# Kernel optimization log

Hardware: AMD Instinct MI355X
Metric: run time of the kernel (lower is better)

The kernel has to match this reference:

```python
import jax, jax.numpy as jnp
import numpy as np
import math

B, D, DCONV = 8192, 1024, 4
MIN_TS, MAX_TS = 10.0, 2000.0


def setup_inputs() -> dict:
    key = jax.random.key(0)
    ks = jax.random.split(key, 9)
    s_in = 1.0 / math.sqrt(D)
    return {
        "x": jax.random.normal(ks[0], (B, D), jnp.float32),
        "h": jax.random.normal(ks[1], (B, D), jnp.float32),
        "conv_buf": jax.random.normal(ks[2], (B, D, DCONV), jnp.float32),
        "W_in": jax.random.uniform(ks[3], (2 * D, D), jnp.float32, -s_in, s_in),
        "b_in": jax.random.uniform(ks[4], (2 * D,), jnp.float32, -s_in, s_in),
        "conv_w": jax.random.uniform(ks[5], (D, DCONV), jnp.float32, -0.5, 0.5),
        "conv_b": jax.random.uniform(ks[6], (D,), jnp.float32, -0.5, 0.5),
        "W_out": jax.random.uniform(ks[7], (D, D), jnp.float32, -s_in, s_in),
        "b_out": jax.random.uniform(ks[8], (D,), jnp.float32, -s_in, s_in),
    }


def _decay(d_model):
    # tau = exp(linspace(log(min_ts), log(max_ts), D)); decay = exp(-1/tau)
    tau = jnp.exp(jnp.linspace(math.log(MIN_TS), math.log(MAX_TS), d_model))
    return jnp.exp(-1.0 / tau)


def reference(x, h, conv_buf, W_in, b_in, conv_w, conv_b, W_out, b_out):
    # in_proj: [B,D] -> [B,2D], split into inner stream and gate
    xz = x @ W_in.T + b_in
    x_inner, z = jnp.split(xz, 2, axis=-1)  # [B,D], [B,D]
    # ring-buffer roll + write newest sample at last slot
    new_buf = jnp.concatenate([conv_buf[:, :, 1:], x_inner[:, :, None]], axis=-1)  # [B,D,K]
    # depthwise conv over the K-window, output length 1
    conv_out = jnp.einsum("bdk,dk->bd", new_buf, conv_w) + conv_b
    conv_out = jax.nn.silu(conv_out)
    # decay-gated recurrence
    decay = _decay(x.shape[-1])
    h_new = decay * h + (1.0 - decay) * conv_out
    # SiLU gate + output projection (dropout is identity in eval)
    out = (h_new * jax.nn.silu(z)) @ W_out.T + b_out
    return out, h_new, new_buf
```

## Files before the change

### kernel.cpp

```cpp
#include <hip/hip_runtime.h>
#include <hip/hip_bf16.h>


typedef float  floatx4 __attribute__((ext_vector_type(4)));
typedef __bf16 bf16x8  __attribute__((ext_vector_type(8)));
typedef unsigned short u16;
typedef unsigned short u16x8 __attribute__((ext_vector_type(8)));

__device__ __forceinline__ float bf2f(u16 u) {
    union { unsigned int i; float f; } v; v.i = ((unsigned int)u) << 16; return v.f;
}
__device__ __forceinline__ u16 f2bf(float f) {
    union { float ff; unsigned int i; } v; v.ff = f;
    return (u16)((v.i + 0x7fffu + ((v.i >> 16) & 1u)) >> 16);
}
__device__ __forceinline__ float silu_f(float x) { return x / (1.f + __expf(-x)); }

#define D_SZ 1024
#define B_SZ 8192
#define ELEMS 8388608
#define WI_ELEMS 2097152
#define WO_ELEMS 1048576

#define WS_XIN 256
#define WS_Z   (WS_XIN + 33554432)
#define WS_XB  (WS_Z + 16777216)
#define WS_WI  (WS_XB + 16777216)
#define WS_WO  (WS_WI + 4194304)

__device__ __forceinline__ void gload_lds16(const void* g, void* l) {
    __builtin_amdgcn_global_load_lds(
        (const __attribute__((address_space(1))) void*)g,
        (__attribute__((address_space(3))) void*)l, 16, 0, 0);
}

__global__ void k_sniff(const u16* __restrict__ x, int* __restrict__ flag) {
    if (threadIdx.x == 0 && blockIdx.x == 0) {
        int bad = 0;
        for (int i = 0; i < 64; ++i) {
            u16 u = x[2 * i];
            int e = (u >> 7) & 0xFF;
            if (e < 64 || e > 160) bad = 1;
        }
        *flag = bad;
    }
}

__global__ __launch_bounds__(256)
void k_convert(const void* __restrict__ xv, const void* __restrict__ wiv,
               const void* __restrict__ wov,
               u16* __restrict__ xb, u16* __restrict__ wib, u16* __restrict__ wob,
               const int* __restrict__ flagp)
{
    const int isf32 = *flagp;
    const int nvec = (ELEMS + WI_ELEMS + WO_ELEMS) / 8;
    for (int i = blockIdx.x * blockDim.x + threadIdx.x; i < nvec;
         i += gridDim.x * blockDim.x) {
        const int e = i * 8;
        const void* src; u16* dst; int off;
        if (e < ELEMS)                 { src = xv;  dst = xb;  off = e; }
        else if (e < ELEMS + WI_ELEMS) { src = wiv; dst = wib; off = e - ELEMS; }
        else                           { src = wov; dst = wob; off = e - ELEMS - WI_ELEMS; }
        if (isf32) {
            const floatx4* s4 = (const floatx4*)((const float*)src + off);
            floatx4 a = s4[0], b = s4[1];
            u16x8 t = { f2bf(a.x), f2bf(a.y), f2bf(a.z), f2bf(a.w),
                        f2bf(b.x), f2bf(b.y), f2bf(b.z), f2bf(b.w) };
            *(u16x8*)(dst + off) = t;
        } else {
            *(u16x8*)(dst + off) = *(const u16x8*)((const u16*)src + off);
        }
    }
}

__device__ __forceinline__ void gemm128_core(const u16* __restrict__ A,
                                             const u16* __restrict__ Bw,
                                             int m0, int n0,
                                             u16* lA, u16* lB,
                                             floatx4 acc[4][4])
{
    const int tid  = threadIdx.x;
    const int lane = tid & 63;
    const int wv   = tid >> 6;
    const int wave_m = wv >> 1, wave_n = wv & 1;
    const int srow = wv * 32 + (lane >> 3);
    const int scol = (lane & 7) * 8;

    for (int kt = 0; kt < 16; ++kt) {
        const int kb = kt * 64;
#pragma unroll
        for (int c = 0; c < 4; ++c) {
            gload_lds16(A  + (size_t)(m0 + srow + c * 8) * D_SZ + kb + scol,
                        &lA[(wv * 4 + c) * 512]);
            gload_lds16(Bw + (size_t)(n0 + srow + c * 8) * D_SZ + kb + scol,
                        &lB[(wv * 4 + c) * 512]);
        }
        __syncthreads();
#pragma unroll
        for (int kk = 0; kk < 2; ++kk) {
            const int kcol = kk * 32 + (lane >> 4) * 8;
            bf16x8 af[4], bfr[4];
#pragma unroll
            for (int i = 0; i < 4; ++i)
                af[i] = *(const bf16x8*)&lA[(wave_m * 64 + i * 16 + (lane & 15)) * 64 + kcol];
#pragma unroll
            for (int j = 0; j < 4; ++j)
                bfr[j] = *(const bf16x8*)&lB[(wave_n * 64 + j * 16 + (lane & 15)) * 64 + kcol];
#pragma unroll
            for (int i = 0; i < 4; ++i)
#pragma unroll
                for (int j = 0; j < 4; ++j)
                    acc[i][j] = __builtin_amdgcn_mfma_f32_16x16x32_bf16(
                        af[i], bfr[j], acc[i][j], 0, 0, 0);
        }
        __syncthreads();
    }
}

__global__ __launch_bounds__(256)
void k_gemm_in(const u16* __restrict__ xb, const u16* __restrict__ wib,
               float* __restrict__ xin, u16* __restrict__ zb)
{
    __shared__ u16 lA[128 * 64];
    __shared__ u16 lB[128 * 64];
    floatx4 acc[4][4];
#pragma unroll
    for (int i = 0; i < 4; ++i)
#pragma unroll
        for (int j = 0; j < 4; ++j) acc[i][j] = (floatx4){0.f, 0.f, 0.f, 0.f};

    const int m0 = blockIdx.x * 128;
    const int n0 = blockIdx.y * 128;
    gemm128_core(xb, wib, m0, n0, lA, lB, acc);

    const int lane = threadIdx.x & 63;
    const int wv   = threadIdx.x >> 6;
    const int wave_m = wv >> 1, wave_n = wv & 1;
    const int col = lane & 15, rgrp = (lane >> 4) * 4;

    if (n0 < D_SZ) {
#pragma unroll
        for (int j = 0; j < 4; ++j) {
            const int n = n0 + wave_n * 64 + j * 16 + col;
#pragma unroll
            for (int i = 0; i < 4; ++i) {
                const int br = m0 + wave_m * 64 + i * 16 + rgrp;
#pragma unroll
                for (int r = 0; r < 4; ++r)
                    xin[(size_t)(br + r) * D_SZ + n] = acc[i][j][r];
            }
        }
    } else {
        const int nz0 = n0 - D_SZ;
#pragma unroll
        for (int j = 0; j < 4; ++j) {
            const int n = nz0 + wave_n * 64 + j * 16 + col;
#pragma unroll
            for (int i = 0; i < 4; ++i) {
                const int br = m0 + wave_m * 64 + i * 16 + rgrp;
#pragma unroll
                for (int r = 0; r < 4; ++r)
                    zb[(size_t)(br + r) * D_SZ + n] = f2bf(acc[i][j][r]);
            }
        }
    }
}

__global__ __launch_bounds__(256)
void k_elem(const float* __restrict__ xin, const u16* __restrict__ zb,
            const void* __restrict__ hv, const void* __restrict__ cbv,
            const void* __restrict__ biv, const void* __restrict__ cwv,
            const void* __restrict__ cbsv, void* __restrict__ outv,
            u16* __restrict__ g, const int* __restrict__ flagp)
{
    const int isf32 = *flagp;
    const u16*     hb  = (const u16*)hv;    const float*   hf  = (const float*)hv;
    const ushort4* cbb = (const ushort4*)cbv; const floatx4* cbf = (const floatx4*)cbv;
    const u16*   bib = (const u16*)biv;   const float*  bif = (const float*)biv;
    const u16*   cwb = (const u16*)cwv;   const float*  cwf = (const float*)cwv;
    const u16*   csb = (const u16*)cbsv;  const float*  csf = (const float*)cbsv;
    u16*   outb = (u16*)outv;   float* outf = (float*)outv;
    u16*     hnb = outb + ELEMS;            float*   hnf = outf + ELEMS;
    ushort4* nbb = (ushort4*)(outb + 2 * ELEMS);
    floatx4* nbf = (floatx4*)(outf + 2 * ELEMS);

    for (int idx = blockIdx.x * blockDim.x + threadIdx.x; idx < ELEMS;
         idx += gridDim.x * blockDim.x) {
        const int d = idx & (D_SZ - 1);
        float binx, binz, w0, w1, w2, w3, cbias, hvv, c1, c2, c3;
        if (isf32) {
            binx = bif[d]; binz = bif[D_SZ + d];
            floatx4 w = *(const floatx4*)(cwf + (size_t)d * 4);
            w0 = w.x; w1 = w.y; w2 = w.z; w3 = w.w;
            cbias = csf[d];
            floatx4 cb = cbf[idx];
            c1 = cb.y; c2 = cb.z; c3 = cb.w;
            hvv = hf[idx];
        } else {
            binx = bf2f(bib[d]); binz = bf2f(bib[D_SZ + d]);
            ushort4 w = *(const ushort4*)(cwb + (size_t)d * 4);
            w0 = bf2f(w.x); w1 = bf2f(w.y); w2 = bf2f(w.z); w3 = bf2f(w.w);
            cbias = bf2f(csb[d]);
            ushort4 cb = cbb[idx];
            c1 = bf2f(cb.y); c2 = bf2f(cb.z); c3 = bf2f(cb.w);
            hvv = bf2f(hb[idx]);
        }
        const float xi = xin[idx] + binx;
        const float zv = bf2f(zb[idx]) + binz;
        const float conv = c1 * w0 + c2 * w1 + c3 * w2 + xi * w3 + cbias;
        const float sc = silu_f(conv);
        const float lin = 2.302585092994046f + (float)d * (5.298317366548036f / 1023.0f);
        const float dec = __expf(-__expf(-lin));
        const float hn = dec * hvv + (1.f - dec) * sc;
        const float gv = hn * silu_f(zv);
        if (isf32) {
            hnf[idx] = hn;
            floatx4 nb = { c1, c2, c3, xi };
            nbf[idx] = nb;
        } else {
            hnb[idx] = f2bf(hn);
            ushort4 nb;
            nb.x = f2bf(c1); nb.y = f2bf(c2); nb.z = f2bf(c3); nb.w = f2bf(xi);
            nbb[idx] = nb;
        }
        g[idx] = f2bf(gv);
    }
}

__global__ __launch_bounds__(256)
void k_gemm_out(const u16* __restrict__ g, const u16* __restrict__ wob,
                const void* __restrict__ bov, void* __restrict__ outv,
                const int* __restrict__ flagp)
{
    __shared__ u16 lA[128 * 64];
    __shared__ u16 lB[128 * 64];
    const int isf32 = *flagp;
    const u16* bb = (const u16*)bov; const float* bf = (const float*)bov;
    u16* outb = (u16*)outv;          float* outf = (float*)outv;

    floatx4 acc[4][4];
#pragma unroll
    for (int i = 0; i < 4; ++i)
#pragma unroll
        for (int j = 0; j < 4; ++j) acc[i][j] = (floatx4){0.f, 0.f, 0.f, 0.f};

    const int m0 = blockIdx.x * 128;
    const int n0 = blockIdx.y * 128;
    gemm128_core(g, wob, m0, n0, lA, lB, acc);

    const int lane = threadIdx.x & 63;
    const int wv   = threadIdx.x >> 6;
    const int wave_m = wv >> 1, wave_n = wv & 1;
    const int col = lane & 15, rgrp = (lane >> 4) * 4;

#pragma unroll
    for (int j = 0; j < 4; ++j) {
        const int n = n0 + wave_n * 64 + j * 16 + col;
        const float bias = isf32 ? bf[n] : bf2f(bb[n]);
#pragma unroll
        for (int i = 0; i < 4; ++i) {
            const int br = m0 + wave_m * 64 + i * 16 + rgrp;
#pragma unroll
            for (int r = 0; r < 4; ++r) {
                const size_t idx = (size_t)(br + r) * D_SZ + n;
                const float v = acc[i][j][r] + bias;
                if (isf32) outf[idx] = v; else outb[idx] = f2bf(v);
            }
        }
    }
}

extern "C" void kernel_launch(void* const* d_in, const int* in_sizes, int n_in,
                              void* d_out, int out_size, void* d_ws, size_t ws_size,
                              hipStream_t stream) {
    const void* x        = d_in[0];
    const void* h        = d_in[1];
    const void* conv_buf = d_in[2];
    const void* W_in     = d_in[3];
    const void* b_in     = d_in[4];
    const void* conv_w   = d_in[5];
    const void* conv_b   = d_in[6];
    const void* W_out    = d_in[7];
    const void* b_out    = d_in[8];

    char* ws = (char*)d_ws;
    int*   flag = (int*)ws;
    float* xin  = (float*)(ws + WS_XIN);
    u16*   zbuf = (u16*)(ws + WS_Z);
    u16*   xbuf = (u16*)(ws + WS_XB);
    u16*   wib  = (u16*)(ws + WS_WI);
    u16*   wob  = (u16*)(ws + WS_WO);
    u16*   gbuf = xbuf;

    k_sniff<<<1, 64, 0, stream>>>((const u16*)x, flag);
    k_convert<<<2048, 256, 0, stream>>>(x, W_in, W_out, xbuf, wib, wob, flag);
    k_gemm_in<<<dim3(64, 16), 256, 0, stream>>>(xbuf, wib, xin, zbuf);
    k_elem<<<2048, 256, 0, stream>>>(xin, zbuf, h, conv_buf, b_in, conv_w,
                                     conv_b, d_out, gbuf, flag);
    k_gemm_out<<<dim3(64, 8), 256, 0, stream>>>(gbuf, wob, b_out, d_out, flag);
}
```

Baseline: 456.2 us.

## Fuse gating/conv elementwise stage into input projection GEMM epilogue

The in-projection GEMM now loads interleaved W_in rows, so each block's tile holds matching x_inner and z columns for the same 32 features per wave. The conv/decay/SiLU-gate math then runs directly on the accumulators. This removes the separate elementwise kernel and the fp32 x_inner and bf16 z intermediates written to and re-read from global memory. In exchange, the epilogue does scattered, per-lane reads of h and conv_buf and writes the outputs with a less coalesced pattern than the old grid-stride loop.

```diff
diff --git a/kernel.cpp b/kernel.cpp
--- a/kernel.cpp
+++ b/kernel.cpp
@@ -22,11 +22,10 @@
 #define WI_ELEMS 2097152
 #define WO_ELEMS 1048576
 
-#define WS_XIN 256
-#define WS_Z   (WS_XIN + 33554432)
-#define WS_XB  (WS_Z + 16777216)
+#define WS_XB  256
 #define WS_WI  (WS_XB + 16777216)
 #define WS_WO  (WS_WI + 4194304)
+#define WS_G   (WS_WO + 2097152)
 
 __device__ __forceinline__ void gload_lds16(const void* g, void* l) {
     __builtin_amdgcn_global_load_lds(
@@ -73,6 +72,134 @@
     }
 }
 
+__global__ __launch_bounds__(256)
+void k1_fused(const u16* __restrict__ xb, const u16* __restrict__ wib,
+              const void* __restrict__ hv, const void* __restrict__ cbv,
+              const void* __restrict__ biv, const void* __restrict__ cwv,
+              const void* __restrict__ cbsv, void* __restrict__ outv,
+              u16* __restrict__ g, const int* __restrict__ flagp)
+{
+    __shared__ u16 lA[128 * 64];
+    __shared__ u16 lB[128 * 64];
+
+    const int isf32 = *flagp;
+    const int tid  = threadIdx.x;
+    const int lane = tid & 63;
+    const int wv   = tid >> 6;
+    const int wave_m = wv >> 1, wave_n = wv & 1;
+    const int m0 = blockIdx.x * 128;
+    const int n0 = blockIdx.y * 64;
+
+    floatx4 acc[4][4];
+#pragma unroll
+    for (int i = 0; i < 4; ++i)
+#pragma unroll
+        for (int j = 0; j < 4; ++j) acc[i][j] = (floatx4){0.f, 0.f, 0.f, 0.f};
+
+    const int srow = wv * 32 + (lane >> 3);
+    const int scol = (lane & 7) * 8;
+
+    for (int kt = 0; kt < 16; ++kt) {
+        const int kb = kt * 64;
+#pragma unroll
+        for (int c = 0; c < 4; ++c) {
+            const int r = srow + c * 8;
+            const int grow = n0 + ((r >> 6) & 1) * 32 + (r & 31) + ((r >> 5) & 1) * 1024;
+            gload_lds16(xb  + (size_t)(m0 + r) * D_SZ + kb + scol,
+                        &lA[(wv * 4 + c) * 512]);
+            gload_lds16(wib + (size_t)grow * D_SZ + kb + scol,
+                        &lB[(wv * 4 + c) * 512]);
+        }
+        __syncthreads();
+#pragma unroll
+        for (int kk = 0; kk < 2; ++kk) {
+            const int kcol = kk * 32 + (lane >> 4) * 8;
+            bf16x8 af[4], bfr[4];
+#pragma unroll
+            for (int i = 0; i < 4; ++i)
+                af[i] = *(const bf16x8*)&lA[(wave_m * 64 + i * 16 + (lane & 15)) * 64 + kcol];
+#pragma unroll
+            for (int j = 0; j < 4; ++j)
+                bfr[j] = *(const bf16x8*)&lB[(wave_n * 64 + j * 16 + (lane & 15)) * 64 + kcol];
+#pragma unroll
+            for (int i = 0; i < 4; ++i)
+#pragma unroll
+                for (int j = 0; j < 4; ++j)
+                    acc[i][j] = __builtin_amdgcn_mfma_f32_16x16x32_bf16(
+                        af[i], bfr[j], acc[i][j], 0, 0, 0);
+        }
+        __syncthreads();
+    }
+
+    const u16*     hb  = (const u16*)hv;      const float*   hf  = (const float*)hv;
+    const ushort4* cbb = (const ushort4*)cbv; const floatx4* cbf = (const floatx4*)cbv;
+    const u16*   bib = (const u16*)biv;   const float*  bif = (const float*)biv;
+    const u16*   cwb = (const u16*)cwv;   const float*  cwf = (const float*)cwv;
+    const u16*   csb = (const u16*)cbsv;  const float*  csf = (const float*)cbsv;
+
+    u16*   outb = (u16*)outv;   float* outf = (float*)outv;
+    u16*     hnb = outb + ELEMS;            float*   hnf = outf + ELEMS;
+    ushort4* nbb = (ushort4*)(outb + 2 * ELEMS);
+    floatx4* nbf = (floatx4*)(outf + 2 * ELEMS);
+
+    const int col  = lane & 15;
+    const int rgrp = (lane >> 4) * 4;
+
+#pragma unroll
+    for (int j = 0; j < 2; ++j) {
+        const int d = n0 + wave_n * 32 + j * 16 + col;
+        float binx, binz, w0, w1, w2, w3, cbias;
+        if (isf32) {
+            binx = bif[d]; binz = bif[D_SZ + d];
+            floatx4 w = *(const floatx4*)(cwf + (size_t)d * 4);
+            w0 = w.x; w1 = w.y; w2 = w.z; w3 = w.w;
+            cbias = csf[d];
+        } else {
+            binx = bf2f(bib[d]); binz = bf2f(bib[D_SZ + d]);
+            ushort4 w4u = *(const ushort4*)&cwb[d * 4];
+            w0 = bf2f(w4u.x); w1 = bf2f(w4u.y); w2 = bf2f(w4u.z); w3 = bf2f(w4u.w);
+            cbias = bf2f(csb[d]);
+        }
+        const float lin = 2.302585092994046f + (float)d * (5.298317366548036f / 1023.0f);
+        const float dec = __expf(-__expf(-lin));
+        const float one_m_dec = 1.f - dec;
+#pragma unroll
+        for (int i = 0; i < 4; ++i) {
+            const int brow = m0 + wave_m * 64 + i * 16 + rgrp;
+#pragma unroll
+            for (int r = 0; r < 4; ++r) {
+                const size_t idx = (size_t)(brow + r) * D_SZ + d;
+                const float xin = acc[i][j][r] + binx;
+                const float zv  = acc[i][j + 2][r] + binz;
+                float c1, c2, c3, hvv;
+                if (isf32) {
+                    floatx4 cb = cbf[idx];
+                    c1 = cb.y; c2 = cb.z; c3 = cb.w;
+                    hvv = hf[idx];
+                } else {
+                    ushort4 cb = cbb[idx];
+                    c1 = bf2f(cb.y); c2 = bf2f(cb.z); c3 = bf2f(cb.w);
+                    hvv = bf2f(hb[idx]);
+                }
+                const float conv = c1 * w0 + c2 * w1 + c3 * w2 + xin * w3 + cbias;
+                const float sc = silu_f(conv);
+                const float hn = dec * hvv + one_m_dec * sc;
+                if (isf32) {
+                    hnf[idx] = hn;
+                    floatx4 nb = { c1, c2, c3, xin };
+                    nbf[idx] = nb;
+                } else {
+                    hnb[idx] = f2bf(hn);
+                    ushort4 nb;
+                    nb.x = f2bf(c1); nb.y = f2bf(c2); nb.z = f2bf(c3); nb.w = f2bf(xin);
+                    nbb[idx] = nb;
+                }
+                g[idx] = f2bf(hn * silu_f(zv));
+            }
+        }
+    }
+}
+
 __device__ __forceinline__ void gemm128_core(const u16* __restrict__ A,
                                              const u16* __restrict__ Bw,
                                              int m0, int n0,
@@ -118,117 +245,7 @@
 }
 
 __global__ __launch_bounds__(256)
-void k_gemm_in(const u16* __restrict__ xb, const u16* __restrict__ wib,
-               float* __restrict__ xin, u16* __restrict__ zb)
-{
-    __shared__ u16 lA[128 * 64];
-    __shared__ u16 lB[128 * 64];
-    floatx4 acc[4][4];
-#pragma unroll
-    for (int i = 0; i < 4; ++i)
-#pragma unroll
-        for (int j = 0; j < 4; ++j) acc[i][j] = (floatx4){0.f, 0.f, 0.f, 0.f};
-
-    const int m0 = blockIdx.x * 128;
-    const int n0 = blockIdx.y * 128;
-    gemm128_core(xb, wib, m0, n0, lA, lB, acc);
-
-    const int lane = threadIdx.x & 63;
-    const int wv   = threadIdx.x >> 6;
-    const int wave_m = wv >> 1, wave_n = wv & 1;
-    const int col = lane & 15, rgrp = (lane >> 4) * 4;
-
-    if (n0 < D_SZ) {
-#pragma unroll
-        for (int j = 0; j < 4; ++j) {
-            const int n = n0 + wave_n * 64 + j * 16 + col;
-#pragma unroll
-            for (int i = 0; i < 4; ++i) {
-                const int br = m0 + wave_m * 64 + i * 16 + rgrp;
-#pragma unroll
-                for (int r = 0; r < 4; ++r)
-                    xin[(size_t)(br + r) * D_SZ + n] = acc[i][j][r];
-            }
-        }
-    } else {
-        const int nz0 = n0 - D_SZ;
-#pragma unroll
-        for (int j = 0; j < 4; ++j) {
-            const int n = nz0 + wave_n * 64 + j * 16 + col;
-#pragma unroll
-            for (int i = 0; i < 4; ++i) {
-                const int br = m0 + wave_m * 64 + i * 16 + rgrp;
-#pragma unroll
-                for (int r = 0; r < 4; ++r)
-                    zb[(size_t)(br + r) * D_SZ + n] = f2bf(acc[i][j][r]);
-            }
-        }
-    }
-}
-
-__global__ __launch_bounds__(256)
-void k_elem(const float* __restrict__ xin, const u16* __restrict__ zb,
-            const void* __restrict__ hv, const void* __restrict__ cbv,
-            const void* __restrict__ biv, const void* __restrict__ cwv,
-            const void* __restrict__ cbsv, void* __restrict__ outv,
-            u16* __restrict__ g, const int* __restrict__ flagp)
-{
-    const int isf32 = *flagp;
-    const u16*     hb  = (const u16*)hv;    const float*   hf  = (const float*)hv;
-    const ushort4* cbb = (const ushort4*)cbv; const floatx4* cbf = (const floatx4*)cbv;
-    const u16*   bib = (const u16*)biv;   const float*  bif = (const float*)biv;
-    const u16*   cwb = (const u16*)cwv;   const float*  cwf = (const float*)cwv;
-    const u16*   csb = (const u16*)cbsv;  const float*  csf = (const float*)cbsv;
-    u16*   outb = (u16*)outv;   float* outf = (float*)outv;
-    u16*     hnb = outb + ELEMS;            float*   hnf = outf + ELEMS;
-    ushort4* nbb = (ushort4*)(outb + 2 * ELEMS);
-    floatx4* nbf = (floatx4*)(outf + 2 * ELEMS);
-
-    for (int idx = blockIdx.x * blockDim.x + threadIdx.x; idx < ELEMS;
-         idx += gridDim.x * blockDim.x) {
-        const int d = idx & (D_SZ - 1);
-        float binx, binz, w0, w1, w2, w3, cbias, hvv, c1, c2, c3;
-        if (isf32) {
-            binx = bif[d]; binz = bif[D_SZ + d];
-            floatx4 w = *(const floatx4*)(cwf + (size_t)d * 4);
-            w0 = w.x; w1 = w.y; w2 = w.z; w3 = w.w;
-            cbias = csf[d];
-            floatx4 cb = cbf[idx];
-            c1 = cb.y; c2 = cb.z; c3 = cb.w;
-            hvv = hf[idx];
-        } else {
-            binx = bf2f(bib[d]); binz = bf2f(bib[D_SZ + d]);
-            ushort4 w = *(const ushort4*)(cwb + (size_t)d * 4);
-            w0 = bf2f(w.x); w1 = bf2f(w.y); w2 = bf2f(w.z); w3 = bf2f(w.w);
-            cbias = bf2f(csb[d]);
-            ushort4 cb = cbb[idx];
-            c1 = bf2f(cb.y); c2 = bf2f(cb.z); c3 = bf2f(cb.w);
-            hvv = bf2f(hb[idx]);
-        }
-        const float xi = xin[idx] + binx;
-        const float zv = bf2f(zb[idx]) + binz;
-        const float conv = c1 * w0 + c2 * w1 + c3 * w2 + xi * w3 + cbias;
-        const float sc = silu_f(conv);
-        const float lin = 2.302585092994046f + (float)d * (5.298317366548036f / 1023.0f);
-        const float dec = __expf(-__expf(-lin));
-        const float hn = dec * hvv + (1.f - dec) * sc;
-        const float gv = hn * silu_f(zv);
-        if (isf32) {
-            hnf[idx] = hn;
-            floatx4 nb = { c1, c2, c3, xi };
-            nbf[idx] = nb;
-        } else {
-            hnb[idx] = f2bf(hn);
-            ushort4 nb;
-            nb.x = f2bf(c1); nb.y = f2bf(c2); nb.z = f2bf(c3); nb.w = f2bf(xi);
-            nbb[idx] = nb;
-        }
-        g[idx] = f2bf(gv);
-    }
-}
-
-__global__ __launch_bounds__(256)
-void k_gemm_out(const u16* __restrict__ g, const u16* __restrict__ wob,
+void k2_outproj(const u16* __restrict__ g, const u16* __restrict__ wob,
                 const void* __restrict__ bov, void* __restrict__ outv,
                 const int* __restrict__ flagp)
 {
@@ -285,17 +302,14 @@
 
     char* ws = (char*)d_ws;
     int*   flag = (int*)ws;
-    float* xin  = (float*)(ws + WS_XIN);
-    u16*   zbuf = (u16*)(ws + WS_Z);
     u16*   xbuf = (u16*)(ws + WS_XB);
     u16*   wib  = (u16*)(ws + WS_WI);
     u16*   wob  = (u16*)(ws + WS_WO);
-    u16*   gbuf = xbuf;
+    u16*   gbuf = (u16*)(ws + WS_G);
 
     k_sniff<<<1, 64, 0, stream>>>((const u16*)x, flag);
     k_convert<<<2048, 256, 0, stream>>>(x, W_in, W_out, xbuf, wib, wob, flag);
-    k_gemm_in<<<dim3(64, 16), 256, 0, stream>>>(xbuf, wib, xin, zbuf);
-    k_elem<<<2048, 256, 0, stream>>>(xin, zbuf, h, conv_buf, b_in, conv_w,
-                                     conv_b, d_out, gbuf, flag);
-    k_gemm_out<<<dim3(64, 8), 256, 0, stream>>>(gbuf, wob, b_out, d_out, flag);
-}
+    k1_fused<<<dim3(64, 16), 256, 0, stream>>>(
+        xbuf, wib, h, conv_buf, b_in, conv_w, conv_b, d_out, gbuf, flag);
+    k2_outproj<<<dim3(64, 8), 256, 0, stream>>>(gbuf, wob, b_out, d_out, flag);
+}
```

Result: slower. 538.7 us (+18.1%).
